# Performance work log

Hardware: AMD Instinct MI355X
Metric: run time of the kernel (lower is better)

## Reference

```python
import jax, jax.numpy as jnp
import numpy as np

N, E, D, H, C, L, G = 50000, 800000, 128, 4, 32, 3, 64  # nodes, edges, hidden, heads, head_dim, layers, graphs


def setup_inputs() -> dict:
    key = jax.random.key(0)
    ks = jax.random.split(key, 20)
    s = 0.05
    inp = {
        "x": jax.random.normal(ks[0], (N, D), jnp.float32),
        "edge_index": jax.random.randint(ks[1], (2, E), 0, N, dtype=jnp.int32),
        "batch": jnp.sort(jax.random.randint(ks[2], (N,), 0, G, dtype=jnp.int32)),
        # input projection
        "W_in": jax.random.normal(ks[3], (D, D), jnp.float32) * s,
        "b_in": jnp.zeros((D,), jnp.float32),
        # stacked per-layer GATConv params
        "lin_W": jax.random.normal(ks[4], (L, D, H * C), jnp.float32) * s,
        "att_src": jax.random.normal(ks[5], (L, H, C), jnp.float32) * s,
        "att_dst": jax.random.normal(ks[6], (L, H, C), jnp.float32) * s,
        "conv_b": jnp.zeros((L, H * C), jnp.float32),
        # stacked LayerNorm params
        "ln_g": jnp.ones((L, D), jnp.float32),
        "ln_b": jnp.zeros((L, D), jnp.float32),
        # output MLP 128 -> 64 -> 1
        "W1": jax.random.normal(ks[7], (D, D // 2), jnp.float32) * s,
        "b1": jnp.zeros((D // 2,), jnp.float32),
        "W2": jax.random.normal(ks[8], (D // 2, 1), jnp.float32) * s,
        "b2": jnp.zeros((1,), jnp.float32),
    }
    return inp


def _layernorm(h, g, b, eps=1e-5):
    mu = jnp.mean(h, axis=-1, keepdims=True)
    var = jnp.var(h, axis=-1, keepdims=True)
    return (h - mu) * jax.lax.rsqrt(var + eps) * g + b


def _gat_conv(x, src, dst, n, W, a_src, a_dst, b):
    # x: [n, D] -> per-head features [n, H, C]
    xh = (x @ W).reshape(n, H, C)
    e_s = jnp.sum(xh * a_src, axis=-1)  # [n, H]
    e_d = jnp.sum(xh * a_dst, axis=-1)  # [n, H]
    e = jax.nn.leaky_relu(e_s[src] + e_d[dst], 0.2)  # [E', H]
    # softmax over incoming edges of each destination node
    m = jax.ops.segment_max(e, dst, num_segments=n)
    ee = jnp.exp(e - m[dst])
    z = jax.ops.segment_sum(ee, dst, num_segments=n)
    alpha = ee / z[dst]
    msg = xh[src] * alpha[:, :, None]  # [E', H, C]
    out = jax.ops.segment_sum(msg, dst, num_segments=n)  # [n, H, C]
    return out.reshape(n, H * C) + b


def reference(x, edge_index, batch, W_in, b_in, lin_W, att_src, att_dst, conv_b, ln_g, ln_b, W1, b1, W2, b2):
    n = x.shape[0]
    # PyG GATConv default add_self_loops=True
    loops = jnp.arange(n, dtype=edge_index.dtype)
    src = jnp.concatenate([edge_index[0], loops])
    dst = jnp.concatenate([edge_index[1], loops])

    h = x @ W_in + b_in
    for l in range(L):
        residual = h
        c = _gat_conv(h, src, dst, n, lin_W[l], att_src[l], att_dst[l], conv_b[l])
        c = _layernorm(c, ln_g[l], ln_b[l])
        h = jax.nn.relu(c) + residual

    # global mean pool over graphs
    sums = jax.ops.segment_sum(h, batch, num_segments=G)
    cnt = jax.ops.segment_sum(jnp.ones((n,), h.dtype), batch, num_segments=G)
    pooled = sums / jnp.maximum(cnt, 1.0)[:, None]

    return jax.nn.relu(pooled @ W1 + b1) @ W2 + b2  # [G, 1]
```

## Files before the change

### kernel.cpp

```cpp
#include <hip/hip_runtime.h>

#define DD 128

typedef __bf16 bf16x8 __attribute__((ext_vector_type(8)));
typedef float  f32x4  __attribute__((ext_vector_type(4)));

__device__ __forceinline__ float lrelu(float x){ return x >= 0.f ? x : 0.2f*x; }
__device__ __forceinline__ float bflo(unsigned u){ return __uint_as_float(u << 16); }
__device__ __forceinline__ float bfhi(unsigned u){ return __uint_as_float(u & 0xffff0000u); }
__device__ __forceinline__ float red16(float v){
  v += __shfl_xor(v,1); v += __shfl_xor(v,2);
  v += __shfl_xor(v,4); v += __shfl_xor(v,8);
  return v;
}

__global__ void k_deg_init(int* deg, int n){
  int i = blockIdx.x*blockDim.x + threadIdx.x;
  if (i < n) deg[i] = 1;
}
__global__ void k_deg_hist(const int* __restrict__ dst, int* __restrict__ deg, int E){
  int base = (blockIdx.x*blockDim.x + threadIdx.x)*4;
  if (base + 4 <= E){
    int4 d = *(const int4*)(dst + base);
    atomicAdd(&deg[d.x], 1);
    atomicAdd(&deg[d.y], 1);
    atomicAdd(&deg[d.z], 1);
    atomicAdd(&deg[d.w], 1);
  } else {
    for (int e = base; e < E; ++e) atomicAdd(&deg[dst[e]], 1);
  }
}
__global__ void k_scan_partial(const int* __restrict__ deg, int* __restrict__ partial, int n){
  __shared__ int s[128];
  int i = blockIdx.x*128 + threadIdx.x;
  int v = (i < n) ? deg[i] : 0;
  s[threadIdx.x] = v; __syncthreads();
  for (int off = 64; off; off >>= 1){
    if (threadIdx.x < off) s[threadIdx.x] += s[threadIdx.x + off];
    __syncthreads();
  }
  if (threadIdx.x == 0) partial[blockIdx.x] = s[0];
}
__global__ void k_scan_top(int* partial, int nChunks){
  __shared__ int s[512];
  int v = (threadIdx.x < nChunks) ? partial[threadIdx.x] : 0;
  s[threadIdx.x] = v; __syncthreads();
  for (int off = 1; off < 512; off <<= 1){
    int t = (threadIdx.x >= (unsigned)off) ? s[threadIdx.x - off] : 0;
    __syncthreads();
    s[threadIdx.x] += t;
    __syncthreads();
  }
  if (threadIdx.x < nChunks) partial[threadIdx.x] = s[threadIdx.x] - v;
}
__global__ void k_scan_final(const int* __restrict__ deg, const int* __restrict__ partial,
                             int* __restrict__ rowptr, int* __restrict__ wptr, int n){
  __shared__ int s[128];
  int i = blockIdx.x*128 + threadIdx.x;
  int v = (i < n) ? deg[i] : 0;
  s[threadIdx.x] = v; __syncthreads();
  for (int off = 1; off < 128; off <<= 1){
    int t = (threadIdx.x >= (unsigned)off) ? s[threadIdx.x - off] : 0;
    __syncthreads();
    s[threadIdx.x] += t;
    __syncthreads();
  }
  int excl = s[threadIdx.x] - v + partial[blockIdx.x];
  if (i < n){
    rowptr[i] = excl; wptr[i] = excl;
    if (i == n-1) rowptr[n] = excl + v;
  }
}
__global__ void k_scatter(const int* __restrict__ src, const int* __restrict__ dst,
                          int* __restrict__ wptr, int* __restrict__ col, int E, int n){
  const int total = E + n;
  int base = (blockIdx.x*blockDim.x + threadIdx.x)*4;
  if (base >= total) return;
  int d[4], s[4]; bool ok[4];
  if (base + 4 <= E){
    int4 dv = *(const int4*)(dst + base);
    int4 sv = *(const int4*)(src + base);
    d[0]=dv.x; d[1]=dv.y; d[2]=dv.z; d[3]=dv.w;
    s[0]=sv.x; s[1]=sv.y; s[2]=sv.z; s[3]=sv.w;
    ok[0]=ok[1]=ok[2]=ok[3]=true;
  } else {
    #pragma unroll
    for (int q = 0; q < 4; ++q){
      int e = base + q;
      ok[q] = e < total;
      if (!ok[q]){ d[q]=0; s[q]=0; }
      else if (e < E){ d[q]=dst[e]; s[q]=src[e]; }
      else { d[q]=e-E; s[q]=e-E; }
    }
  }
  int p[4];
  #pragma unroll
  for (int q = 0; q < 4; ++q) if (ok[q]) p[q] = atomicAdd(&wptr[d[q]], 1);
  #pragma unroll
  for (int q = 0; q < 4; ++q) if (ok[q]) col[p[q]] = s[q];
}

__global__ void k_wprep(const float* __restrict__ Win, const float* __restrict__ linW,
                        __bf16* __restrict__ wt){
  int idx = blockIdx.x*256 + threadIdx.x;
  int m = idx >> 14, r = idx & 16383;
  int k = r >> 7, c = r & 127;
  const float* src = (m == 0) ? Win : linW + (size_t)(m-1)*DD*DD;
  float w = src[(size_t)k*DD + c];
  __bf16 hi = (__bf16)w;
  __bf16 lo = (__bf16)(w - (float)hi);
  wt[(size_t)(2*m  )*DD*DD + (size_t)c*DD + k] = hi;
  wt[(size_t)(2*m+1)*DD*DD + (size_t)c*DD + k] = lo;
}

template<int OUTF32>
__global__ __launch_bounds__(256) void k_mm_mfma(const float* __restrict__ hin,
    const __bf16* __restrict__ Wt, const float* __restrict__ bias,
    float* __restrict__ outf, __bf16* __restrict__ outb,
    const float* __restrict__ att_s, const float* __restrict__ att_d,
    float* __restrict__ es, float* __restrict__ ed, int n, int N)
{
  const int tid = threadIdx.x;
  const int wv  = tid >> 6, l = tid & 63;
  const int lr = l & 15, lk = l >> 4;
  const int row0 = blockIdx.x*32 + (wv >> 1)*16;
  const int ct0  = (wv & 1)*4;
  int arow = row0 + lr; if (arow >= n) arow = n - 1;
  const float* hp = hin + (size_t)arow*DD + lk*8;
  bf16x8 ah[4], al[4];
  #pragma unroll
  for (int kc = 0; kc < 4; ++kc){
    float4 lo4 = *(const float4*)(hp + kc*32);
    float4 hi4 = *(const float4*)(hp + kc*32 + 4);
    float vv[8] = {lo4.x,lo4.y,lo4.z,lo4.w,hi4.x,hi4.y,hi4.z,hi4.w};
    bf16x8 vh, vl;
    #pragma unroll
    for (int q = 0; q < 8; ++q){
      __bf16 h = (__bf16)vv[q];
      vh[q] = h;
      vl[q] = (__bf16)(vv[q] - (float)h);
    }
    ah[kc] = vh; al[kc] = vl;
  }
  f32x4 acc[4];
  #pragma unroll
  for (int ct = 0; ct < 4; ++ct) acc[ct] = (f32x4){0.f,0.f,0.f,0.f};
  const __bf16* wp = Wt + (size_t)lr*DD + lk*8;
  #pragma unroll
  for (int ct = 0; ct < 4; ++ct){
    const __bf16* wpc = wp + (size_t)(ct0+ct)*16*DD;
    #pragma unroll
    for (int kc = 0; kc < 4; ++kc){
      bf16x8 bh = *(const bf16x8*)(wpc + (size_t)kc*32);
      bf16x8 bl = *(const bf16x8*)(wpc + DD*DD + (size_t)kc*32);
      acc[ct] = __builtin_amdgcn_mfma_f32_16x16x32_bf16(ah[kc], bh, acc[ct], 0, 0, 0);
      acc[ct] = __builtin_amdgcn_mfma_f32_16x16x32_bf16(al[kc], bh, acc[ct], 0, 0, 0);
      acc[ct] = __builtin_amdgcn_mfma_f32_16x16x32_bf16(ah[kc], bl, acc[ct], 0, 0, 0);
    }
  }
  const int orow0 = row0 + lk*4;
  #pragma unroll
  for (int ct = 0; ct < 4; ++ct){
    const int colc = (ct0+ct)*16 + lr;
    float badd = 0.f;
    if (OUTF32) badd = bias[colc];
    #pragma unroll
    for (int q = 0; q < 4; ++q){
      int row = orow0 + q;
      if (row < n){
        if (OUTF32) outf[(size_t)row*DD + colc] = acc[ct][q] + badd;
        else        outb[(size_t)row*DD + colc] = (__bf16)acc[ct][q];
      }
    }
  }
  if (!OUTF32){
    float as4[4], ad4[4];
    #pragma unroll
    for (int ct = 0; ct < 4; ++ct){
      int colc = (ct0+ct)*16 + lr;
      as4[ct] = att_s[colc];
      ad4[ct] = att_d[colc];
    }
    float psA[4], psB[4], pdA[4], pdB[4];
    #pragma unroll
    for (int q = 0; q < 4; ++q){
      psA[q] = red16(acc[0][q]*as4[0] + acc[1][q]*as4[1]);
      psB[q] = red16(acc[2][q]*as4[2] + acc[3][q]*as4[3]);
      pdA[q] = red16(acc[0][q]*ad4[0] + acc[1][q]*ad4[1]);
      pdB[q] = red16(acc[2][q]*ad4[2] + acc[3][q]*ad4[3]);
    }
    if (lr == 0){
      const int hA = ct0 >> 1, hB = hA + 1;
      #pragma unroll
      for (int q = 0; q < 4; ++q){
        int row = orow0 + q;
        if (row < n){
          es[(size_t)hA*N + row] = psA[q];
          es[(size_t)hB*N + row] = psB[q];
          ed[(size_t)hA*N + row] = pdA[q];
          ed[(size_t)hB*N + row] = pdB[q];
        }
      }
    }
  }
}

__global__ __launch_bounds__(256) void k_agg(const unsigned* __restrict__ xp,
    const float* __restrict__ es, const float* __restrict__ ed,
    const int* __restrict__ rowptr, const int* __restrict__ col,
    const float* __restrict__ cb, const float* __restrict__ lg, const float* __restrict__ lb,
    float* __restrict__ h, int n, int N)
{
  int wid = (blockIdx.x * blockDim.x + threadIdx.x) >> 6;
  int lane = threadIdx.x & 63;
  if (wid >= n) return;
  const int i = wid;
  const int rs = rowptr[i], re = rowptr[i+1];
  const int hsel = lane >> 4;
  const float* esh = es + (size_t)hsel*N;
  const float edd = ed[(size_t)hsel*N + i];
  float z = 0.f, a0 = 0.f, a1 = 0.f;
  const int slast = col[re-1];
  for (int j = rs; j < re; j += 8){
    int s[8]; bool ok[8];
    #pragma unroll
    for (int q = 0; q < 8; ++q){
      int jq = j + q;
      ok[q] = jq < re;
      s[q] = ok[q] ? col[jq] : slast;
    }
    float e[8]; unsigned u[8];
    #pragma unroll
    for (int q = 0; q < 8; ++q) e[q] = esh[s[q]];
    #pragma unroll
    for (int q = 0; q < 8; ++q) u[q] = xp[(size_t)s[q]*64 + lane];
    #pragma unroll
    for (int q = 0; q < 8; ++q){
      float w = ok[q] ? __expf(lrelu(e[q] + edd)) : 0.f;
      z += w;
      a0 = fmaf(bflo(u[q]), w, a0);
      a1 = fmaf(bfhi(u[q]), w, a1);
    }
  }
  float zi = 1.f / z;
  float2 cbv = *(const float2*)(cb + 2*lane);
  float c0 = a0*zi + cbv.x;
  float c1 = a1*zi + cbv.y;
  float sum = c0 + c1, sq = c0*c0 + c1*c1;
  #pragma unroll
  for (int off = 1; off < 64; off <<= 1){
    sum += __shfl_xor(sum, off);
    sq  += __shfl_xor(sq,  off);
  }
  float mu  = sum * (1.f/128.f);
  float var = sq  * (1.f/128.f) - mu*mu;
  float rinv = rsqrtf(var + 1e-5f);
  float2 lgv = *(const float2*)(lg + 2*lane);
  float2 lbv = *(const float2*)(lb + 2*lane);
  float y0 = (c0 - mu)*rinv*lgv.x + lbv.x;
  float y1 = (c1 - mu)*rinv*lgv.y + lbv.y;
  float2 rv = *(const float2*)(h + (size_t)i*DD + 2*lane);
  float2 o;
  o.x = fmaxf(y0, 0.f) + rv.x;
  o.y = fmaxf(y1, 0.f) + rv.y;
  *(float2*)(h + (size_t)i*DD + 2*lane) = o;
}

__global__ void k_pool(const float* __restrict__ h, const int* __restrict__ batch,
                       float* __restrict__ pooled, float* __restrict__ cnt, int n){
  int d = threadIdx.x;
  int n0 = blockIdx.x * 8;
  if (n0 >= n) return;
  int n1 = min(n0 + 8, n);
  float acc = 0.f, cacc = 0.f; int cur = batch[n0];
  for (int i = n0; i < n1; ++i){
    int g = batch[i];
    float v = h[(size_t)i*DD + d];
    if (g != cur){
      atomicAdd(&pooled[cur*DD + d], acc);
      if (d == 0) atomicAdd(&cnt[cur], cacc);
      acc = 0.f; cacc = 0.f; cur = g;
    }
    acc += v;
    cacc += 1.f;
  }
  atomicAdd(&pooled[cur*DD + d], acc);
  if (d == 0) atomicAdd(&cnt[cur], cacc);
}

__global__ void k_mlp(const float* __restrict__ pooled, const float* __restrict__ cnt,
                      const float* __restrict__ W1, const float* __restrict__ b1,
                      const float* __restrict__ W2, const float* __restrict__ b2,
                      float* __restrict__ out, int G_){
  int g = blockIdx.x, lane = threadIdx.x;
  float inv = 1.f / fmaxf(cnt[g], 1.f);
  float acc = b1[lane];
  for (int k = 0; k < DD; ++k)
    acc = fmaf(pooled[g*DD + k]*inv, W1[k*64 + lane], acc);
  float hv = fmaxf(acc, 0.f) * W2[lane];
  #pragma unroll
  for (int off = 32; off; off >>= 1) hv += __shfl_down(hv, off);
  if (lane == 0) out[g] = hv + b2[0];
}

extern "C" void kernel_launch(void* const* d_in, const int* in_sizes, int n_in,
                              void* d_out, int out_size, void* d_ws, size_t ws_size,
                              hipStream_t stream){
  const float* x       = (const float*)d_in[0];
  const int*   ei      = (const int*)d_in[1];
  const int*   batch   = (const int*)d_in[2];
  const float* W_in    = (const float*)d_in[3];
  const float* b_in    = (const float*)d_in[4];
  const float* lin_W   = (const float*)d_in[5];
  const float* att_src = (const float*)d_in[6];
  const float* att_dst = (const float*)d_in[7];
  const float* conv_b  = (const float*)d_in[8];
  const float* ln_g    = (const float*)d_in[9];
  const float* ln_b    = (const float*)d_in[10];
  const float* W1      = (const float*)d_in[11];
  const float* b1      = (const float*)d_in[12];
  const float* W2      = (const float*)d_in[13];
  const float* b2      = (const float*)d_in[14];
  float* outp = (float*)d_out;

  const int N = in_sizes[0] / DD;
  const int E = in_sizes[1] / 2;
  const int G = out_size;
  const int L = 3;
  const int* srcp = ei;
  const int* dstp = ei + E;

  size_t off = 0;
  auto alloc = [&](size_t bytes) -> void* {
    void* p = (char*)d_ws + off;
    off += (bytes + 255) & ~(size_t)255;
    return p;
  };
  float*  h      = (float*) alloc((size_t)N*DD*4);
  __bf16* xhb    = (__bf16*)alloc((size_t)N*DD*2);
  float*  es     = (float*) alloc((size_t)N*4*4);
  float*  ed     = (float*) alloc((size_t)N*4*4);
  int*    deg    = (int*)   alloc((size_t)N*4);
  int*    rowptr = (int*)   alloc((size_t)(N+1)*4);
  int*    wptr   = (int*)   alloc((size_t)(N+1)*4);
  int*    col    = (int*)   alloc((size_t)(E+N)*4);
  int*    partial= (int*)   alloc(512*4);
  __bf16* wt     = (__bf16*)alloc((size_t)8*DD*DD*2);
  float*  pooled = (float*) alloc((size_t)G*DD*4);
  float*  cnt    = (float*) alloc((size_t)G*4);

  const int nChunks = (N + 127)/128;

  k_deg_init<<<(N+255)/256, 256, 0, stream>>>(deg, N);
  k_deg_hist<<<(E/4+255)/256, 256, 0, stream>>>(dstp, deg, E);
  k_scan_partial<<<nChunks, 128, 0, stream>>>(deg, partial, N);
  k_scan_top<<<1, 512, 0, stream>>>(partial, nChunks);
  k_scan_final<<<nChunks, 128, 0, stream>>>(deg, partial, rowptr, wptr, N);
  k_scatter<<<((E+N)/4+255)/256, 256, 0, stream>>>(srcp, dstp, wptr, col, E, N);

  k_wprep<<<256, 256, 0, stream>>>(W_in, lin_W, wt);

  k_mm_mfma<1><<<(N+31)/32, 256, 0, stream>>>(x, wt, b_in, h, nullptr,
                                              nullptr, nullptr, nullptr, nullptr, N, N);

  for (int l = 0; l < L; ++l){
    k_mm_mfma<0><<<(N+31)/32, 256, 0, stream>>>(h, wt + (size_t)2*(1+l)*DD*DD, nullptr,
                                                nullptr, xhb,
                                                att_src + l*DD, att_dst + l*DD, es, ed, N, N);
    k_agg<<<(N+3)/4, 256, 0, stream>>>((const unsigned*)xhb, es, ed, rowptr, col,
                                       conv_b + l*DD, ln_g + l*DD, ln_b + l*DD, h, N, N);
  }

  hipMemsetAsync(pooled, 0, (size_t)G*DD*4, stream);
  hipMemsetAsync(cnt,    0, (size_t)G*4,    stream);
  k_pool<<<(N+7)/8, 128, 0, stream>>>(h, batch, pooled, cnt, N);
  k_mlp<<<G, 64, 0, stream>>>(pooled, cnt, W1, b1, W2, b2, outp, G);
}
```

Before: 534.4 us.

## Split each wavefront into four edge groups with 16-byte feature gathers

The aggregation kernel now splits each 64-lane wavefront into four groups of 16 lanes. Each group handles a different edge and each lane loads 16 bytes (8 bf16 features) instead of 4 bytes. Partial sums are combined across the groups with cross-lane shuffles, and LayerNorm is reduced within 16 lanes. The aim is fewer, wider gather instructions and more edges in flight per wave, at the cost of more registers and extra shuffle reductions.

```diff
diff --git a/kernel.cpp b/kernel.cpp
--- a/kernel.cpp
+++ b/kernel.cpp
@@ -216,54 +216,71 @@
   if (wid >= n) return;
   const int i = wid;
   const int rs = rowptr[i], re = rowptr[i+1];
-  const int hsel = lane >> 4;
+  const int eq  = lane >> 4;
+  const int l16 = lane & 15;
+  const int hsel = l16 >> 2;
   const float* esh = es + (size_t)hsel*N;
   const float edd = ed[(size_t)hsel*N + i];
-  float z = 0.f, a0 = 0.f, a1 = 0.f;
+  float z = 0.f;
+  float a0=0.f,a1=0.f,a2=0.f,a3=0.f,a4=0.f,a5=0.f,a6=0.f,a7=0.f;
   const int slast = col[re-1];
   for (int j = rs; j < re; j += 8){
-    int s[8]; bool ok[8];
-    #pragma unroll
-    for (int q = 0; q < 8; ++q){
-      int jq = j + q;
-      ok[q] = jq < re;
-      s[q] = ok[q] ? col[jq] : slast;
-    }
-    float e[8]; unsigned u[8];
-    #pragma unroll
-    for (int q = 0; q < 8; ++q) e[q] = esh[s[q]];
-    #pragma unroll
-    for (int q = 0; q < 8; ++q) u[q] = xp[(size_t)s[q]*64 + lane];
-    #pragma unroll
-    for (int q = 0; q < 8; ++q){
-      float w = ok[q] ? __expf(lrelu(e[q] + edd)) : 0.f;
+    #pragma unroll
+    for (int u2 = 0; u2 < 2; ++u2){
+      int jq = j + 4*u2 + eq;
+      bool ok = jq < re;
+      int s = ok ? col[jq] : slast;
+      uint4 u = *(const uint4*)(xp + (size_t)s*64 + 4*l16);
+      float e = esh[s];
+      float w = ok ? __expf(lrelu(e + edd)) : 0.f;
       z += w;
-      a0 = fmaf(bflo(u[q]), w, a0);
-      a1 = fmaf(bfhi(u[q]), w, a1);
-    }
-  }
+      a0 = fmaf(bflo(u.x), w, a0); a1 = fmaf(bfhi(u.x), w, a1);
+      a2 = fmaf(bflo(u.y), w, a2); a3 = fmaf(bfhi(u.y), w, a3);
+      a4 = fmaf(bflo(u.z), w, a4); a5 = fmaf(bfhi(u.z), w, a5);
+      a6 = fmaf(bflo(u.w), w, a6); a7 = fmaf(bfhi(u.w), w, a7);
+    }
+  }
+  z  += __shfl_xor(z,16);  z  += __shfl_xor(z,32);
+  a0 += __shfl_xor(a0,16); a0 += __shfl_xor(a0,32);
+  a1 += __shfl_xor(a1,16); a1 += __shfl_xor(a1,32);
+  a2 += __shfl_xor(a2,16); a2 += __shfl_xor(a2,32);
+  a3 += __shfl_xor(a3,16); a3 += __shfl_xor(a3,32);
+  a4 += __shfl_xor(a4,16); a4 += __shfl_xor(a4,32);
+  a5 += __shfl_xor(a5,16); a5 += __shfl_xor(a5,32);
+  a6 += __shfl_xor(a6,16); a6 += __shfl_xor(a6,32);
+  a7 += __shfl_xor(a7,16); a7 += __shfl_xor(a7,32);
   float zi = 1.f / z;
-  float2 cbv = *(const float2*)(cb + 2*lane);
-  float c0 = a0*zi + cbv.x;
-  float c1 = a1*zi + cbv.y;
-  float sum = c0 + c1, sq = c0*c0 + c1*c1;
-  #pragma unroll
-  for (int off = 1; off < 64; off <<= 1){
+  float4 cb0 = *(const float4*)(cb + 8*l16);
+  float4 cb1 = *(const float4*)(cb + 8*l16 + 4);
+  float c0 = a0*zi + cb0.x, c1 = a1*zi + cb0.y, c2 = a2*zi + cb0.z, c3 = a3*zi + cb0.w;
+  float c4 = a4*zi + cb1.x, c5 = a5*zi + cb1.y, c6 = a6*zi + cb1.z, c7 = a7*zi + cb1.w;
+  float sum = ((c0+c1)+(c2+c3)) + ((c4+c5)+(c6+c7));
+  float sq  = (c0*c0+c1*c1+c2*c2+c3*c3) + (c4*c4+c5*c5+c6*c6+c7*c7);
+  #pragma unroll
+  for (int off = 1; off < 16; off <<= 1){
     sum += __shfl_xor(sum, off);
     sq  += __shfl_xor(sq,  off);
   }
   float mu  = sum * (1.f/128.f);
   float var = sq  * (1.f/128.f) - mu*mu;
   float rinv = rsqrtf(var + 1e-5f);
-  float2 lgv = *(const float2*)(lg + 2*lane);
-  float2 lbv = *(const float2*)(lb + 2*lane);
-  float y0 = (c0 - mu)*rinv*lgv.x + lbv.x;
-  float y1 = (c1 - mu)*rinv*lgv.y + lbv.y;
-  float2 rv = *(const float2*)(h + (size_t)i*DD + 2*lane);
-  float2 o;
-  o.x = fmaxf(y0, 0.f) + rv.x;
-  o.y = fmaxf(y1, 0.f) + rv.y;
-  *(float2*)(h + (size_t)i*DD + 2*lane) = o;
+  if (eq == 0){
+    float4 lg0 = *(const float4*)(lg + 8*l16), lg1 = *(const float4*)(lg + 8*l16 + 4);
+    float4 lb0 = *(const float4*)(lb + 8*l16), lb1 = *(const float4*)(lb + 8*l16 + 4);
+    float4 r0 = *(const float4*)(h + (size_t)i*DD + 8*l16);
+    float4 r1 = *(const float4*)(h + (size_t)i*DD + 8*l16 + 4);
+    float4 o0, o1;
+    o0.x = fmaxf((c0-mu)*rinv*lg0.x + lb0.x, 0.f) + r0.x;
+    o0.y = fmaxf((c1-mu)*rinv*lg0.y + lb0.y, 0.f) + r0.y;
+    o0.z = fmaxf((c2-mu)*rinv*lg0.z + lb0.z, 0.f) + r0.z;
+    o0.w = fmaxf((c3-mu)*rinv*lg0.w + lb0.w, 0.f) + r0.w;
+    o1.x = fmaxf((c4-mu)*rinv*lg1.x + lb1.x, 0.f) + r1.x;
+    o1.y = fmaxf((c5-mu)*rinv*lg1.y + lb1.y, 0.f) + r1.y;
+    o1.z = fmaxf((c6-mu)*rinv*lg1.z + lb1.z, 0.f) + r1.z;
+    o1.w = fmaxf((c7-mu)*rinv*lg1.w + lb1.w, 0.f) + r1.w;
+    *(float4*)(h + (size_t)i*DD + 8*l16)     = o0;
+    *(float4*)(h + (size_t)i*DD + 8*l16 + 4) = o1;
+  }
 }
 
 __global__ void k_pool(const float* __restrict__ h, const int* __restrict__ batch,
```

After: 546.4 us. 2.2% more time.
